# Kernel tuning notes

Hardware: AMD Instinct MI355X
Metric: run time of the kernel (lower is better)

Reference implementation:

```python
import jax, jax.numpy as jnp
import numpy as np

B, C, H, W = 2, 192, 256, 256
HEADS = 6


def _conv1x1(x, w, b):
    # x: [b,ci,h,w], w: [co,ci,1,1], b: [co]
    return jnp.einsum('oi,bihw->bohw', w[:, :, 0, 0], x) + b[None, :, None, None]


def _dwconv3x3(x, w, b):
    # depthwise 3x3, padding=1; x: [b,c,h,w], w: [c,1,3,3], b: [c]
    y = jax.lax.conv_general_dilated(
        x, w, window_strides=(1, 1), padding='SAME',
        feature_group_count=x.shape[1],
        dimension_numbers=('NCHW', 'OIHW', 'NCHW'))
    return y + b[None, :, None, None]


def _l2norm(t, eps=1e-12):
    # F.normalize(dim=-1): x / max(||x||_2, eps)
    n = jnp.sqrt(jnp.sum(t * t, axis=-1, keepdims=True))
    return t / jnp.maximum(n, eps)


def setup_inputs() -> dict:
    key = jax.random.key(0)
    ks = jax.random.split(key, 12)
    s = 0.02
    return {
        'feat_guide': jax.random.normal(ks[0], (B, C, H, W), jnp.float32),
        'feat_op': jax.random.normal(ks[1], (B, C, H, W), jnp.float32),
        'q_w': jax.random.normal(ks[2], (C, C, 1, 1), jnp.float32) * s,
        'q_b': jax.random.normal(ks[3], (C,), jnp.float32) * s,
        'kv_w': jax.random.normal(ks[4], (2 * C, C, 1, 1), jnp.float32) * s,
        'kv_b': jax.random.normal(ks[5], (2 * C,), jnp.float32) * s,
        'q_dw_w': jax.random.normal(ks[6], (C, 1, 3, 3), jnp.float32) * s,
        'q_dw_b': jax.random.normal(ks[7], (C,), jnp.float32) * s,
        'kv_dw_w': jax.random.normal(ks[8], (2 * C, 1, 3, 3), jnp.float32) * s,
        'kv_dw_b': jax.random.normal(ks[9], (2 * C,), jnp.float32) * s,
        'proj_w': jax.random.normal(ks[10], (C, C, 1, 1), jnp.float32) * s,
        'proj_b': jax.random.normal(ks[11], (C,), jnp.float32) * s,
        'temperature': jnp.ones((HEADS, 1, 1), jnp.float32),
    }


def reference(feat_guide, feat_op, q_w, q_b, kv_w, kv_b, q_dw_w, q_dw_b,
              kv_dw_w, kv_dw_b, proj_w, proj_b, temperature):
    b, c, h, w = feat_guide.shape
    q = _dwconv3x3(_conv1x1(feat_guide, q_w, q_b), q_dw_w, q_dw_b)
    kv = _dwconv3x3(_conv1x1(feat_op, kv_w, kv_b), kv_dw_w, kv_dw_b)
    k, v = jnp.split(kv, 2, axis=1)

    def heads(t):  # [b,c,h,w] -> [b,heads,c/heads,hw]
        return t.reshape(b, HEADS, c // HEADS, h * w)

    q = _l2norm(heads(q))
    k = _l2norm(heads(k))
    v = heads(v)
    # channel-wise attention: [b,heads,c',c'] scores over hw
    attn = jnp.einsum('bhcn,bhdn->bhcd', q, k) * temperature[None]
    attn = jax.nn.softmax(attn, axis=-1)
    out = jnp.einsum('bhcd,bhdn->bhcn', attn, v).reshape(b, c, h, w)
    return _conv1x1(out, proj_w, proj_b)
```

## Files before the change

kernel.cpp:

```cpp
#include <hip/hip_runtime.h>

#define HW_N 65536
#define CC 192
#define NCHUNKS 256

typedef __attribute__((ext_vector_type(8))) short short8v;
typedef __attribute__((ext_vector_type(4))) short short4v;
typedef __attribute__((ext_vector_type(4))) float f32x4;
typedef __attribute__((ext_vector_type(4))) int int4v;

__device__ __forceinline__ float bf2f(unsigned short u) {
  union { unsigned int i; float f; } v; v.i = ((unsigned int)u) << 16; return v.f;
}
__device__ __forceinline__ unsigned short f2bf(float f) {
  union { float f; unsigned int i; } v; v.f = f;
  unsigned int r = v.i + 0x7fffu + ((v.i >> 16) & 1u);
  return (unsigned short)(r >> 16);
}

__global__ __launch_bounds__(256) void cvt_w(
    const float* __restrict__ qw, const float* __restrict__ kvw,
    unsigned short* __restrict__ Wq, unsigned short* __restrict__ Wkv) {
  const int i = (blockIdx.x * 256 + threadIdx.x) * 8;
  const float* src; unsigned short* dst; int off;
  if (i < 36864) { src = qw; dst = Wq; off = i; }
  else { src = kvw; dst = Wkv; off = i - 36864; }
  unsigned short tmp[8];
#pragma unroll
  for (int j = 0; j < 8; ++j) tmp[j] = f2bf(src[off + j]);
  *(short8v*)(dst + off) = *(short8v*)tmp;
}

template <int INF32, int OUTF32>
__device__ __forceinline__ void gemm_body(
    const void* __restrict__ X_, const unsigned short* __restrict__ W,
    const float* __restrict__ bias, void* __restrict__ out_,
    int Mtot, int m0, int n0, int b, int t, unsigned char* smem) {
  typedef unsigned short row200[200];
  typedef unsigned short row152[152];
  row200* Bt = (row200*)smem;
  row152* Rp = (row152*)smem;
  const int lane = t & 63, wv = t >> 6;
  const int l15 = lane & 15, lg = lane >> 4;
  const int wm = wv & 3, wn = wv >> 2;
  const int mrow = m0 + wm * 48;
  const int nw = wn * 64;
  const size_t xbase = (size_t)b * CC * (size_t)HW_N + n0;

  for (int task = t; task < 768; task += 512) {
    const int kp = task >> 5, nq = task & 31;
    unsigned int p[8][2];
    if (INF32) {
      const float* Xf = (const float*)X_;
#pragma unroll
      for (int j = 0; j < 8; ++j) {
        f32x4 v = *(const f32x4*)(Xf + xbase + (size_t)(kp * 8 + j) * HW_N + nq * 4);
        p[j][0] = (unsigned int)f2bf(v[0]) | ((unsigned int)f2bf(v[1]) << 16);
        p[j][1] = (unsigned int)f2bf(v[2]) | ((unsigned int)f2bf(v[3]) << 16);
      }
    } else {
      const unsigned short* Xh = (const unsigned short*)X_;
#pragma unroll
      for (int j = 0; j < 8; ++j) {
        short4v v = *(const short4v*)(Xh + xbase + (size_t)(kp * 8 + j) * HW_N + nq * 4);
        p[j][0] = (unsigned int)(unsigned short)v[0] | ((unsigned int)(unsigned short)v[1] << 16);
        p[j][1] = (unsigned int)(unsigned short)v[2] | ((unsigned int)(unsigned short)v[3] << 16);
      }
    }
    const int kpx = kp ^ (nq & 7);
#pragma unroll
    for (int nn = 0; nn < 4; ++nn) {
      unsigned int q4[4];
#pragma unroll
      for (int wi = 0; wi < 4; ++wi) {
        const unsigned int lo = (p[2 * wi][nn >> 1] >> ((nn & 1) * 16)) & 0xffffu;
        const unsigned int hi = (p[2 * wi + 1][nn >> 1] >> ((nn & 1) * 16)) & 0xffffu;
        q4[wi] = lo | (hi << 16);
      }
      *(int4v*)&Bt[nq * 4 + nn][kpx * 8] = *(int4v*)q4;
    }
  }
  __syncthreads();

  f32x4 acc[3][4] = {};
#pragma unroll
  for (int kc = 0; kc < 6; ++kc) {
    const int k0 = kc * 32 + lg * 8;
    short8v af[3], bfr[4];
#pragma unroll
    for (int fr = 0; fr < 3; ++fr)
      af[fr] = *(const short8v*)(W + (size_t)(mrow + fr * 16 + l15) * CC + k0);
#pragma unroll
    for (int fc = 0; fc < 4; ++fc) {
      const int row = nw + fc * 16 + l15;
      const int oct = (kc * 4 + lg) ^ ((row >> 2) & 7);
      bfr[fc] = *(const short8v*)&Bt[row][oct * 8];
    }
#pragma unroll
    for (int fr = 0; fr < 3; ++fr)
#pragma unroll
      for (int fc = 0; fc < 4; ++fc)
        acc[fr][fc] = __builtin_amdgcn_mfma_f32_16x16x32_bf16(af[fr], bfr[fc], acc[fr][fc], 0, 0, 0);
  }

  const size_t obase = (size_t)b * Mtot * (size_t)HW_N;
  if (OUTF32) {
    float* outf = (float*)out_;
#pragma unroll
    for (int fr = 0; fr < 3; ++fr) {
      const int rbase = mrow + fr * 16 + lg * 4;
#pragma unroll
      for (int r = 0; r < 4; ++r) {
        const float bb = bias[rbase + r];
        const size_t ro = obase + (size_t)(rbase + r) * HW_N + n0 + nw;
#pragma unroll
        for (int fc = 0; fc < 4; ++fc)
          outf[ro + fc * 16 + l15] = acc[fr][fc][r] + bb;
      }
    }
    return;
  }
  __syncthreads();

#pragma unroll
  for (int half = 0; half < 2; ++half) {
    if ((wm >> 1) == half) {
      const int mbase = (wm & 1) * 48;
#pragma unroll
      for (int fr = 0; fr < 3; ++fr) {
#pragma unroll
        for (int r = 0; r < 4; ++r) {
          const int mloc = mbase + fr * 16 + lg * 4 + r;
          const float bb = bias[m0 + half * 96 + mloc];
#pragma unroll
          for (int fc = 0; fc < 4; ++fc)
            Rp[mloc][nw + fc * 16 + l15] = f2bf(acc[fr][fc][r] + bb);
        }
      }
    }
    __syncthreads();
#pragma unroll
    for (int s = 0; s < 3; ++s) {
      const int idx = s * 512 + t;
      const int m = idx >> 4, n8 = (idx & 15) * 8;
      short8v v = *(short8v*)&Rp[m][n8];
      const size_t oo = obase + (size_t)(m0 + half * 96 + m) * HW_N + n0 + n8;
      *(short8v*)((unsigned short*)out_ + oo) = v;
    }
    __syncthreads();
  }
}

__global__ __launch_bounds__(512) void conv_gemm_qkv(
    const float* __restrict__ fg, const float* __restrict__ fo,
    const unsigned short* __restrict__ Wq, const unsigned short* __restrict__ Wkv,
    const float* __restrict__ q_b, const float* __restrict__ kv_b,
    unsigned short* __restrict__ QC, unsigned short* __restrict__ KVC) {
  __shared__ __align__(16) unsigned char smem[51200];
  const int d = blockIdx.x;
  const int b = blockIdx.z;
  const int t = threadIdx.x;
  if (d < 512) {
    gemm_body<1, 0>((const void*)fg, Wq, q_b, (void*)QC, 192, 0, d * 128, b, t, smem);
  } else {
    const int dd = d - 512;
    const int mt = (dd >> 3) & 1;
    const int nt = (dd & 7) | ((dd >> 4) << 3);
    gemm_body<1, 0>((const void*)fo, Wkv, kv_b, (void*)KVC, 384, mt * 192, nt * 128, b, t, smem);
  }
}

__global__ __launch_bounds__(512) void conv_gemm_final(
    const unsigned short* __restrict__ Vb, const unsigned short* __restrict__ Mw,
    const float* __restrict__ proj_b, float* __restrict__ out) {
  __shared__ __align__(16) unsigned char smem[51200];
  const int b = blockIdx.z;
  gemm_body<0, 1>((const void*)Vb, Mw + (size_t)b * CC * CC, proj_b, (void*)out,
                  192, 0, blockIdx.x * 128, b, threadIdx.x, smem);
}

__global__ __launch_bounds__(256) void dwconv3x3_all(
    const unsigned short* __restrict__ QC, const unsigned short* __restrict__ KVC,
    const float* __restrict__ q_dw_w, const float* __restrict__ q_dw_b,
    const float* __restrict__ kv_dw_w, const float* __restrict__ kv_dw_b,
    unsigned short* __restrict__ Qb, unsigned short* __restrict__ Kb,
    unsigned short* __restrict__ Vb) {
  const int t = threadIdx.x;
  const int wc = (t & 31) * 8;
  const int h0 = blockIdx.x * 32 + (t >> 5) * 4;
  const int y = blockIdx.y, b = blockIdx.z;
  const unsigned short* in; const float* w; float bv; unsigned short* out;
  if (y < 192) {
    in = QC + ((size_t)b * 192 + y) * (size_t)HW_N;
    w = q_dw_w + y * 9; bv = q_dw_b[y];
    out = Qb + ((size_t)b * 192 + y) * (size_t)HW_N;
  } else if (y < 384) {
    const int c = y - 192;
    in = KVC + ((size_t)b * 384 + c) * (size_t)HW_N;
    w = kv_dw_w + c * 9; bv = kv_dw_b[c];
    out = Kb + ((size_t)b * 192 + c) * (size_t)HW_N;
  } else {
    const int c = y - 384;
    in = KVC + ((size_t)b * 384 + 192 + c) * (size_t)HW_N;
    w = kv_dw_w + (192 + c) * 9; bv = kv_dw_b[192 + c];
    out = Vb + ((size_t)b * 192 + c) * (size_t)HW_N;
  }
  float wv9[9];
#pragma unroll
  for (int i = 0; i < 9; ++i) wv9[i] = w[i];
  float f[6][10];
#pragma unroll
  for (int ky = 0; ky < 6; ++ky) {
    const int hh = h0 + ky - 1;
    if (hh < 0 || hh > 255) {
#pragma unroll
      for (int j = 0; j < 10; ++j) f[ky][j] = 0.f;
    } else {
      const unsigned short* row = in + hh * 256;
      short8v v = *(const short8v*)(row + wc);
      f[ky][0] = (wc > 0) ? bf2f(row[wc - 1]) : 0.f;
#pragma unroll
      for (int j = 0; j < 8; ++j) f[ky][1 + j] = bf2f((unsigned short)v[j]);
      f[ky][9] = (wc < 248) ? bf2f(row[wc + 8]) : 0.f;
    }
  }
#pragma unroll
  for (int rr = 0; rr < 4; ++rr) {
    union { short8v v; unsigned short u[8]; } o;
#pragma unroll
    for (int j = 0; j < 8; ++j) {
      float acc = bv;
#pragma unroll
      for (int ky = 0; ky < 3; ++ky)
#pragma unroll
        for (int kx = 0; kx < 3; ++kx)
          acc += wv9[ky * 3 + kx] * f[rr + ky][j + kx];
      o.u[j] = f2bf(acc);
    }
    *(short8v*)(out + (h0 + rr) * 256 + wc) = o.v;
  }
}

__global__ __launch_bounds__(64) void gram_kernel(
    const unsigned short* __restrict__ Q, const unsigned short* __restrict__ K,
    float* __restrict__ Gp, float* __restrict__ nqp, float* __restrict__ nkp) {
  const int lane = threadIdx.x;
  const int l15 = lane & 15, lg = lane >> 4;
  const int chunk = blockIdx.x, h = blockIdx.y, b = blockIdx.z;
  const int bh = b * 6 + h;
  const size_t base = ((size_t)b * CC + h * 32) * (size_t)HW_N;
  f32x4 acc[2][2] = {};
  float sq[2] = {0.f, 0.f}, sk[2] = {0.f, 0.f};
  const int nst = chunk * 256 + lg * 8;
  for (int ks = 0; ks < 8; ++ks) {
    const int n = nst + ks * 32;
    short8v qa[2], kb[2];
#pragma unroll
    for (int fr = 0; fr < 2; ++fr) {
      qa[fr] = *(const short8v*)(Q + base + (size_t)(fr * 16 + l15) * HW_N + n);
      kb[fr] = *(const short8v*)(K + base + (size_t)(fr * 16 + l15) * HW_N + n);
    }
#pragma unroll
    for (int fr = 0; fr < 2; ++fr)
#pragma unroll
      for (int j = 0; j < 8; ++j) {
        float a = bf2f((unsigned short)qa[fr][j]); sq[fr] += a * a;
        float c2 = bf2f((unsigned short)kb[fr][j]); sk[fr] += c2 * c2;
      }
#pragma unroll
    for (int fr = 0; fr < 2; ++fr)
#pragma unroll
      for (int fc = 0; fc < 2; ++fc)
        acc[fr][fc] = __builtin_amdgcn_mfma_f32_16x16x32_bf16(qa[fr], kb[fc], acc[fr][fc], 0, 0, 0);
  }
  float* Gb = Gp + (size_t)(chunk * 12 + bh) * 1024;
#pragma unroll
  for (int fr = 0; fr < 2; ++fr)
#pragma unroll
    for (int fc = 0; fc < 2; ++fc)
#pragma unroll
      for (int r = 0; r < 4; ++r)
        Gb[(fr * 16 + lg * 4 + r) * 32 + fc * 16 + l15] = acc[fr][fc][r];
#pragma unroll
  for (int fr = 0; fr < 2; ++fr) {
    float v = sq[fr]; v += __shfl_down(v, 32); v += __shfl_down(v, 16);
    float u = sk[fr]; u += __shfl_down(u, 32); u += __shfl_down(u, 16);
    if (lane < 16) {
      nqp[(size_t)(chunk * 12 + bh) * 32 + fr * 16 + lane] = v;
      nkp[(size_t)(chunk * 12 + bh) * 32 + fr * 16 + lane] = u;
    }
  }
}

__global__ __launch_bounds__(256) void attn_proj_fused(
    const float* __restrict__ Gp, const float* __restrict__ nqp, const float* __restrict__ nkp,
    const float* __restrict__ temp, const float* __restrict__ proj_w,
    unsigned short* __restrict__ Mout) {
  const int h = blockIdx.x, b = blockIdx.y;
  const int bh = b * 6 + h;
  const int t = threadIdx.x;
  __shared__ float sc[32][33];
  __shared__ float nrmq[32], nrmk[32];

  f32x4 gs = {0.f, 0.f, 0.f, 0.f};
  const float* gbase = Gp + (size_t)bh * 1024 + t * 4;
  for (int ch = 0; ch < NCHUNKS; ++ch) {
    f32x4 v = *(const f32x4*)(gbase + (size_t)ch * 12288);
    gs[0] += v[0]; gs[1] += v[1]; gs[2] += v[2]; gs[3] += v[3];
  }
  {
    const int c = t >> 3, d0 = (t * 4) & 31;
#pragma unroll
    for (int j = 0; j < 4; ++j) sc[c][d0 + j] = gs[j];
  }
  if (t < 64) {
    const float* np = (t < 32 ? nqp : nkp) + (size_t)bh * 32 + (t & 31);
    float s = 0.f;
    for (int ch = 0; ch < NCHUNKS; ++ch) s += np[(size_t)ch * 384];
    if (t < 32) nrmq[t] = fmaxf(sqrtf(s), 1e-12f);
    else nrmk[t - 32] = fmaxf(sqrtf(s), 1e-12f);
  }
  __syncthreads();
  const float tpr = temp[h];
  for (int i = t; i < 1024; i += 256) {
    const int c = i >> 5, d = i & 31;
    sc[c][d] = sc[c][d] * tpr / (nrmq[c] * nrmk[d]);
  }
  __syncthreads();
  if (t < 32) {
    float mx = -1e30f;
    for (int d = 0; d < 32; ++d) mx = fmaxf(mx, sc[t][d]);
    float sum = 0.f;
    for (int d = 0; d < 32; ++d) { float e = __expf(sc[t][d] - mx); sc[t][d] = e; sum += e; }
    const float inv = 1.f / sum;
    for (int d = 0; d < 32; ++d) sc[t][d] *= inv;
  }
  __syncthreads();
  for (int i = t; i < 6144; i += 256) {
    const int co = i >> 5, d = i & 31;
    float acc = 0.f;
    for (int c = 0; c < 32; ++c) acc += proj_w[co * CC + h * 32 + c] * sc[c][d];
    Mout[((size_t)b * CC + co) * CC + h * 32 + d] = f2bf(acc);
  }
}

extern "C" void kernel_launch(void* const* d_in, const int* in_sizes, int n_in,
                              void* d_out, int out_size, void* d_ws, size_t ws_size,
                              hipStream_t stream) {
  const float* fg = (const float*)d_in[0];
  const float* fo = (const float*)d_in[1];
  const float* q_w = (const float*)d_in[2];
  const float* q_b = (const float*)d_in[3];
  const float* kv_w = (const float*)d_in[4];
  const float* kv_b = (const float*)d_in[5];
  const float* q_dw_w = (const float*)d_in[6];
  const float* q_dw_b = (const float*)d_in[7];
  const float* kv_dw_w = (const float*)d_in[8];
  const float* kv_dw_b = (const float*)d_in[9];
  const float* proj_w = (const float*)d_in[10];
  const float* proj_b = (const float*)d_in[11];
  const float* temp = (const float*)d_in[12];

  char* ws = (char*)d_ws;
  unsigned short* QC  = (unsigned short*)(ws + 0);
  unsigned short* KVC = (unsigned short*)(ws + 50331648);
  unsigned short* Qb  = (unsigned short*)(ws + 150994944);
  unsigned short* Kb  = (unsigned short*)(ws + 0);
  unsigned short* Vb  = (unsigned short*)(ws + 50331648);
  float* Gp  = (float*)(ws + 100663296);
  float* nqp = (float*)(ws + 113246208);
  float* nkp = (float*)(ws + 113639424);
  unsigned short* Mw  = (unsigned short*)(ws + 208063488);
  unsigned short* Wq  = (unsigned short*)(ws + 208210944);
  unsigned short* Wkv = (unsigned short*)(ws + 208284672);

  cvt_w<<<dim3(54), dim3(256), 0, stream>>>(q_w, kv_w, Wq, Wkv);
  conv_gemm_qkv<<<dim3(1536, 1, 2), dim3(512), 0, stream>>>(
      fg, fo, Wq, Wkv, q_b, kv_b, QC, KVC);
  dwconv3x3_all<<<dim3(8, 576, 2), dim3(256), 0, stream>>>(
      QC, KVC, q_dw_w, q_dw_b, kv_dw_w, kv_dw_b, Qb, Kb, Vb);
  gram_kernel<<<dim3(NCHUNKS, 6, 2), dim3(64), 0, stream>>>(Qb, Kb, Gp, nqp, nkp);
  attn_proj_fused<<<dim3(6, 2), dim3(256), 0, stream>>>(
      Gp, nqp, nkp, temp, proj_w, Mw);
  conv_gemm_final<<<dim3(512, 1, 2), dim3(512), 0, stream>>>(Vb, Mw, proj_b, (float*)d_out);
}
```

Baseline: 266.9 us.

## Fuse Q/K depthwise conv into Gram kernel via shared-memory row tiles

Computes the Q and K depthwise 3x3 convolutions for two image rows per block into LDS and feeds them straight into the MFMA Gram and norm accumulation, so the Q and K intermediates are never written to or re-read from global memory. Each block reduces its four wave partials in LDS and writes one partial per row pair, which halves the number of partial chunks. V still gets its own depthwise kernel. The trailing __syncthreads in the GEMM body is skipped on the second half. The costs are that each block rereads its 3-row halo from global memory and that the Gram blocks are much larger, with more LDS and register pressure.

Result: slower. 294.6 us (+10.4%).

```diff
diff --git a/kernel.cpp b/kernel.cpp
--- a/kernel.cpp
+++ b/kernel.cpp
@@ -2,7 +2,7 @@
 
 #define HW_N 65536
 #define CC 192
-#define NCHUNKS 256
+#define GCHUNKS 128
 
 typedef __attribute__((ext_vector_type(8))) short short8v;
 typedef __attribute__((ext_vector_type(4))) short short4v;
@@ -147,7 +147,7 @@
       const size_t oo = obase + (size_t)(m0 + half * 96 + m) * HW_N + n0 + n8;
       *(short8v*)((unsigned short*)out_ + oo) = v;
     }
-    __syncthreads();
+    if (half == 0) __syncthreads();
   }
 }
 
@@ -179,32 +179,17 @@
                   192, 0, blockIdx.x * 128, b, threadIdx.x, smem);
 }
 
-__global__ __launch_bounds__(256) void dwconv3x3_all(
-    const unsigned short* __restrict__ QC, const unsigned short* __restrict__ KVC,
-    const float* __restrict__ q_dw_w, const float* __restrict__ q_dw_b,
-    const float* __restrict__ kv_dw_w, const float* __restrict__ kv_dw_b,
-    unsigned short* __restrict__ Qb, unsigned short* __restrict__ Kb,
-    unsigned short* __restrict__ Vb) {
+__global__ __launch_bounds__(256) void dwconv3x3_v(
+    const unsigned short* __restrict__ KVC, const float* __restrict__ kv_dw_w,
+    const float* __restrict__ kv_dw_b, unsigned short* __restrict__ Vb) {
   const int t = threadIdx.x;
   const int wc = (t & 31) * 8;
   const int h0 = blockIdx.x * 32 + (t >> 5) * 4;
-  const int y = blockIdx.y, b = blockIdx.z;
-  const unsigned short* in; const float* w; float bv; unsigned short* out;
-  if (y < 192) {
-    in = QC + ((size_t)b * 192 + y) * (size_t)HW_N;
-    w = q_dw_w + y * 9; bv = q_dw_b[y];
-    out = Qb + ((size_t)b * 192 + y) * (size_t)HW_N;
-  } else if (y < 384) {
-    const int c = y - 192;
-    in = KVC + ((size_t)b * 384 + c) * (size_t)HW_N;
-    w = kv_dw_w + c * 9; bv = kv_dw_b[c];
-    out = Kb + ((size_t)b * 192 + c) * (size_t)HW_N;
-  } else {
-    const int c = y - 384;
-    in = KVC + ((size_t)b * 384 + 192 + c) * (size_t)HW_N;
-    w = kv_dw_w + (192 + c) * 9; bv = kv_dw_b[192 + c];
-    out = Vb + ((size_t)b * 192 + c) * (size_t)HW_N;
-  }
+  const int c = blockIdx.y, b = blockIdx.z;
+  const unsigned short* in = KVC + ((size_t)b * 384 + 192 + c) * (size_t)HW_N;
+  const float* w = kv_dw_w + (192 + c) * 9;
+  const float bv = kv_dw_b[192 + c];
+  unsigned short* out = Vb + ((size_t)b * CC + c) * (size_t)HW_N;
   float wv9[9];
 #pragma unroll
   for (int i = 0; i < 9; ++i) wv9[i] = w[i];
@@ -241,54 +226,132 @@
   }
 }
 
-__global__ __launch_bounds__(64) void gram_kernel(
-    const unsigned short* __restrict__ Q, const unsigned short* __restrict__ K,
+__global__ __launch_bounds__(256) void dwgram(
+    const unsigned short* __restrict__ QC, const unsigned short* __restrict__ KVC,
+    const float* __restrict__ q_dw_w, const float* __restrict__ q_dw_b,
+    const float* __restrict__ kv_dw_w, const float* __restrict__ kv_dw_b,
     float* __restrict__ Gp, float* __restrict__ nqp, float* __restrict__ nkp) {
-  const int lane = threadIdx.x;
+  __shared__ __align__(16) unsigned char smem[33280];
+  typedef unsigned short row260[260];
+  row260* Qs = (row260*)smem;
+  row260* Ks = (row260*)(smem + 16640);
+  float* Pp = (float*)smem;
+  float* Np = (float*)(smem + 16640);
+  const int t = threadIdx.x;
+  const int rp = blockIdx.x, h = blockIdx.y, b = blockIdx.z;
+  const int bh = b * 6 + h;
+  const int lane = t & 63, wv = t >> 6;
   const int l15 = lane & 15, lg = lane >> 4;
-  const int chunk = blockIdx.x, h = blockIdx.y, b = blockIdx.z;
-  const int bh = b * 6 + h;
-  const size_t base = ((size_t)b * CC + h * 32) * (size_t)HW_N;
+
   f32x4 acc[2][2] = {};
   float sq[2] = {0.f, 0.f}, sk[2] = {0.f, 0.f};
-  const int nst = chunk * 256 + lg * 8;
-  for (int ks = 0; ks < 8; ++ks) {
-    const int n = nst + ks * 32;
-    short8v qa[2], kb[2];
-#pragma unroll
-    for (int fr = 0; fr < 2; ++fr) {
-      qa[fr] = *(const short8v*)(Q + base + (size_t)(fr * 16 + l15) * HW_N + n);
-      kb[fr] = *(const short8v*)(K + base + (size_t)(fr * 16 + l15) * HW_N + n);
-    }
-#pragma unroll
-    for (int fr = 0; fr < 2; ++fr)
+
+  for (int rr2 = 0; rr2 < 2; ++rr2) {
+    const int r = rp * 2 + rr2;
+#pragma unroll
+    for (int it = 0; it < 8; ++it) {
+      const int tid = it * 256 + t;
+      const int tensor = tid >> 10;
+      const int c = (tid >> 5) & 31;
+      const int g = tid & 31;
+      const int ch = h * 32 + c;
+      const unsigned short* src = tensor == 0
+          ? QC + ((size_t)b * CC + ch) * (size_t)HW_N
+          : KVC + ((size_t)b * 384 + ch) * (size_t)HW_N;
+      const float* wp = (tensor == 0 ? q_dw_w : kv_dw_w) + ch * 9;
+      const float bv = (tensor == 0 ? q_dw_b : kv_dw_b)[ch];
+      float wv9[9];
+#pragma unroll
+      for (int i = 0; i < 9; ++i) wv9[i] = wp[i];
+      const int w0 = g * 8;
+      float f[3][10];
+#pragma unroll
+      for (int ky = 0; ky < 3; ++ky) {
+        const int rimg = r + ky - 1;
+        if (rimg < 0 || rimg > 255) {
+#pragma unroll
+          for (int j = 0; j < 10; ++j) f[ky][j] = 0.f;
+        } else {
+          const unsigned short* row = src + rimg * 256;
+          short8v v = *(const short8v*)(row + w0);
+          f[ky][0] = (w0 > 0) ? bf2f(row[w0 - 1]) : 0.f;
+#pragma unroll
+          for (int j = 0; j < 8; ++j) f[ky][1 + j] = bf2f((unsigned short)v[j]);
+          f[ky][9] = (w0 < 248) ? bf2f(row[w0 + 8]) : 0.f;
+        }
+      }
+      union { short8v v; unsigned short u[8]; } o;
 #pragma unroll
       for (int j = 0; j < 8; ++j) {
-        float a = bf2f((unsigned short)qa[fr][j]); sq[fr] += a * a;
-        float c2 = bf2f((unsigned short)kb[fr][j]); sk[fr] += c2 * c2;
-      }
-#pragma unroll
-    for (int fr = 0; fr < 2; ++fr)
-#pragma unroll
-      for (int fc = 0; fc < 2; ++fc)
-        acc[fr][fc] = __builtin_amdgcn_mfma_f32_16x16x32_bf16(qa[fr], kb[fc], acc[fr][fc], 0, 0, 0);
-  }
-  float* Gb = Gp + (size_t)(chunk * 12 + bh) * 1024;
+        float a = bv;
+#pragma unroll
+        for (int ky = 0; ky < 3; ++ky)
+#pragma unroll
+          for (int kx = 0; kx < 3; ++kx)
+            a += wv9[ky * 3 + kx] * f[ky][j + kx];
+        o.u[j] = f2bf(a);
+      }
+      if (tensor == 0) *(short8v*)&Qs[c][w0] = o.v;
+      else *(short8v*)&Ks[c][w0] = o.v;
+    }
+    __syncthreads();
+
+#pragma unroll
+    for (int s = 0; s < 2; ++s) {
+      const int px = (wv * 2 + s) * 32 + lg * 8;
+      short8v qa[2], kb[2];
+#pragma unroll
+      for (int fr = 0; fr < 2; ++fr) {
+        qa[fr] = *(const short8v*)&Qs[fr * 16 + l15][px];
+        kb[fr] = *(const short8v*)&Ks[fr * 16 + l15][px];
+      }
+#pragma unroll
+      for (int fr = 0; fr < 2; ++fr)
+#pragma unroll
+        for (int j = 0; j < 8; ++j) {
+          float a = bf2f((unsigned short)qa[fr][j]); sq[fr] += a * a;
+          float c2 = bf2f((unsigned short)kb[fr][j]); sk[fr] += c2 * c2;
+        }
+#pragma unroll
+      for (int fr = 0; fr < 2; ++fr)
+#pragma unroll
+        for (int fc = 0; fc < 2; ++fc)
+          acc[fr][fc] = __builtin_amdgcn_mfma_f32_16x16x32_bf16(qa[fr], kb[fc], acc[fr][fc], 0, 0, 0);
+    }
+    __syncthreads();
+  }
+
 #pragma unroll
   for (int fr = 0; fr < 2; ++fr)
 #pragma unroll
     for (int fc = 0; fc < 2; ++fc)
 #pragma unroll
-      for (int r = 0; r < 4; ++r)
-        Gb[(fr * 16 + lg * 4 + r) * 32 + fc * 16 + l15] = acc[fr][fc][r];
+      for (int rr = 0; rr < 4; ++rr)
+        Pp[wv * 1024 + (fr * 16 + lg * 4 + rr) * 32 + fc * 16 + l15] = acc[fr][fc][rr];
 #pragma unroll
   for (int fr = 0; fr < 2; ++fr) {
     float v = sq[fr]; v += __shfl_down(v, 32); v += __shfl_down(v, 16);
     float u = sk[fr]; u += __shfl_down(u, 32); u += __shfl_down(u, 16);
     if (lane < 16) {
-      nqp[(size_t)(chunk * 12 + bh) * 32 + fr * 16 + lane] = v;
-      nkp[(size_t)(chunk * 12 + bh) * 32 + fr * 16 + lane] = u;
-    }
+      Np[wv * 64 + fr * 16 + lane] = v;
+      Np[wv * 64 + 32 + fr * 16 + lane] = u;
+    }
+  }
+  __syncthreads();
+
+  {
+    f32x4 s = {0.f, 0.f, 0.f, 0.f};
+#pragma unroll
+    for (int w = 0; w < 4; ++w) {
+      f32x4 v = *(const f32x4*)&Pp[w * 1024 + t * 4];
+      s[0] += v[0]; s[1] += v[1]; s[2] += v[2]; s[3] += v[3];
+    }
+    *(f32x4*)&Gp[(size_t)(rp * 12 + bh) * 1024 + t * 4] = s;
+  }
+  if (t < 64) {
+    const float s = Np[t] + Np[64 + t] + Np[128 + t] + Np[192 + t];
+    if (t < 32) nqp[(size_t)(rp * 12 + bh) * 32 + t] = s;
+    else nkp[(size_t)(rp * 12 + bh) * 32 + (t - 32)] = s;
   }
 }
 
@@ -304,7 +367,7 @@
 
   f32x4 gs = {0.f, 0.f, 0.f, 0.f};
   const float* gbase = Gp + (size_t)bh * 1024 + t * 4;
-  for (int ch = 0; ch < NCHUNKS; ++ch) {
+  for (int ch = 0; ch < GCHUNKS; ++ch) {
     f32x4 v = *(const f32x4*)(gbase + (size_t)ch * 12288);
     gs[0] += v[0]; gs[1] += v[1]; gs[2] += v[2]; gs[3] += v[3];
   }
@@ -316,7 +379,7 @@
   if (t < 64) {
     const float* np = (t < 32 ? nqp : nkp) + (size_t)bh * 32 + (t & 31);
     float s = 0.f;
-    for (int ch = 0; ch < NCHUNKS; ++ch) s += np[(size_t)ch * 384];
+    for (int ch = 0; ch < GCHUNKS; ++ch) s += np[(size_t)ch * 384];
     if (t < 32) nrmq[t] = fmaxf(sqrtf(s), 1e-12f);
     else nrmk[t - 32] = fmaxf(sqrtf(s), 1e-12f);
   }
@@ -364,22 +427,21 @@
   char* ws = (char*)d_ws;
   unsigned short* QC  = (unsigned short*)(ws + 0);
   unsigned short* KVC = (unsigned short*)(ws + 50331648);
-  unsigned short* Qb  = (unsigned short*)(ws + 150994944);
-  unsigned short* Kb  = (unsigned short*)(ws + 0);
-  unsigned short* Vb  = (unsigned short*)(ws + 50331648);
-  float* Gp  = (float*)(ws + 100663296);
-  float* nqp = (float*)(ws + 113246208);
-  float* nkp = (float*)(ws + 113639424);
-  unsigned short* Mw  = (unsigned short*)(ws + 208063488);
-  unsigned short* Wq  = (unsigned short*)(ws + 208210944);
-  unsigned short* Wkv = (unsigned short*)(ws + 208284672);
+  unsigned short* Vb  = (unsigned short*)(ws + 150994944);
+  float* Gp  = (float*)(ws + 201326592);
+  float* nqp = (float*)(ws + 207618048);
+  float* nkp = (float*)(ws + 207814656);
+  unsigned short* Mw  = (unsigned short*)(ws + 208011264);
+  unsigned short* Wq  = (unsigned short*)(ws + 208158720);
+  unsigned short* Wkv = (unsigned short*)(ws + 208232448);
 
   cvt_w<<<dim3(54), dim3(256), 0, stream>>>(q_w, kv_w, Wq, Wkv);
   conv_gemm_qkv<<<dim3(1536, 1, 2), dim3(512), 0, stream>>>(
       fg, fo, Wq, Wkv, q_b, kv_b, QC, KVC);
-  dwconv3x3_all<<<dim3(8, 576, 2), dim3(256), 0, stream>>>(
-      QC, KVC, q_dw_w, q_dw_b, kv_dw_w, kv_dw_b, Qb, Kb, Vb);
-  gram_kernel<<<dim3(NCHUNKS, 6, 2), dim3(64), 0, stream>>>(Qb, Kb, Gp, nqp, nkp);
+  dwgram<<<dim3(GCHUNKS, 6, 2), dim3(256), 0, stream>>>(
+      QC, KVC, q_dw_w, q_dw_b, kv_dw_w, kv_dw_b, Gp, nqp, nkp);
+  dwconv3x3_v<<<dim3(8, 192, 2), dim3(256), 0, stream>>>(
+      KVC, kv_dw_w, kv_dw_b, Vb);
   attn_proj_fused<<<dim3(6, 2), dim3(256), 0, stream>>>(
       Gp, nqp, nkp, temp, proj_w, Mw);
   conv_gemm_final<<<dim3(512, 1, 2), dim3(512), 0, stream>>>(Vb, Mw, proj_b, (float*)d_out);
```

## Specialize QKV conv GEMM with async global-to-LDS double-buffered fp32 loads

Applied to the files above, without the earlier changes.

Replaces the generic gemm_body call in the QKV 1x1-conv kernel with a specialized body. Activation tiles are streamed as fp32 directly into LDS via global_load_lds with an XOR swizzle and two buffers, while weights are read from global memory straight into registers. The fp32-to-bf16 conversion moves into the fragment build, and LDS use drops to 32 KB, which may raise occupancy. It also removes the trailing barrier after the last epilogue half. In exchange, the loop does more per-element conversion work and carries extra barrier pairs per k-chunk.

Measured after the change: 265.4 us. No clear change (-0.6%).

```diff
diff --git a/kernel.cpp b/kernel.cpp
--- a/kernel.cpp
+++ b/kernel.cpp
@@ -147,7 +147,7 @@
       const size_t oo = obase + (size_t)(m0 + half * 96 + m) * HW_N + n0 + n8;
       *(short8v*)((unsigned short*)out_ + oo) = v;
     }
-    __syncthreads();
+    if (half == 0) __syncthreads();
   }
 }
 
@@ -156,17 +156,102 @@
     const unsigned short* __restrict__ Wq, const unsigned short* __restrict__ Wkv,
     const float* __restrict__ q_b, const float* __restrict__ kv_b,
     unsigned short* __restrict__ QC, unsigned short* __restrict__ KVC) {
-  __shared__ __align__(16) unsigned char smem[51200];
+  __shared__ __align__(16) unsigned char smem[32768];
+  typedef unsigned short row152[152];
+  row152* Rp = (row152*)smem;
   const int d = blockIdx.x;
   const int b = blockIdx.z;
   const int t = threadIdx.x;
-  if (d < 512) {
-    gemm_body<1, 0>((const void*)fg, Wq, q_b, (void*)QC, 192, 0, d * 128, b, t, smem);
-  } else {
+  const float* X; const unsigned short* W; const float* bias; unsigned short* out;
+  int Mtot, m0, n0;
+  if (d < 512) { X = fg; W = Wq; bias = q_b; out = QC; Mtot = 192; m0 = 0; n0 = d * 128; }
+  else {
     const int dd = d - 512;
     const int mt = (dd >> 3) & 1;
     const int nt = (dd & 7) | ((dd >> 4) << 3);
-    gemm_body<1, 0>((const void*)fo, Wkv, kv_b, (void*)KVC, 384, mt * 192, nt * 128, b, t, smem);
+    X = fo; W = Wkv; bias = kv_b; out = KVC; Mtot = 384; m0 = mt * 192; n0 = nt * 128;
+  }
+  const int lane = t & 63, wv = t >> 6;
+  const int l15 = lane & 15, lg = lane >> 4;
+  const int wm = wv & 3, wn = wv >> 2;
+  const int mrow = m0 + wm * 48;
+  const int nw = wn * 64;
+  const size_t xbase = (size_t)b * CC * (size_t)HW_N + n0;
+
+  auto issue = [&](int kc) {
+    const int bsel = kc & 1;
+#pragma unroll
+    for (int i = 0; i < 2; ++i) {
+      const int blk = wv * 2 + i;
+      const int kl = blk * 2 + (lane >> 5);
+      const int g = (lane & 31) ^ (((kl >> 3) & 1) << 2);
+      const float* gp = X + xbase + (size_t)(kc * 32 + kl) * HW_N + g * 4;
+      __builtin_amdgcn_global_load_lds(
+          (const __attribute__((address_space(1))) void*)gp,
+          (__attribute__((address_space(3))) void*)(smem + bsel * 16384 + blk * 1024),
+          16, 0, 0);
+    }
+  };
+
+  issue(0);
+  issue(1);
+
+  f32x4 acc[3][4] = {};
+  for (int kc = 0; kc < 6; ++kc) {
+    __syncthreads();
+    const float* buf = (const float*)(smem + (kc & 1) * 16384);
+    short8v af[3], bfr[4];
+    const int k0 = kc * 32 + lg * 8;
+#pragma unroll
+    for (int fr = 0; fr < 3; ++fr)
+      af[fr] = *(const short8v*)(W + (size_t)(mrow + fr * 16 + l15) * CC + k0);
+#pragma unroll
+    for (int fc = 0; fc < 4; ++fc) {
+      const int nn = nw + fc * 16 + l15;
+      const int sg = (((nn >> 2) ^ ((lg & 1) << 2)) << 2) + (nn & 3);
+      unsigned short u[8];
+#pragma unroll
+      for (int j = 0; j < 8; ++j)
+        u[j] = f2bf(buf[(lg * 8 + j) * 128 + sg]);
+      bfr[fc] = *(short8v*)u;
+    }
+    __syncthreads();
+    if (kc < 4) issue(kc + 2);
+#pragma unroll
+    for (int fr = 0; fr < 3; ++fr)
+#pragma unroll
+      for (int fc = 0; fc < 4; ++fc)
+        acc[fr][fc] = __builtin_amdgcn_mfma_f32_16x16x32_bf16(af[fr], bfr[fc], acc[fr][fc], 0, 0, 0);
+  }
+
+  const size_t obase = (size_t)b * Mtot * (size_t)HW_N;
+  __syncthreads();
+#pragma unroll
+  for (int half = 0; half < 2; ++half) {
+    if ((wm >> 1) == half) {
+      const int mbase = (wm & 1) * 48;
+#pragma unroll
+      for (int fr = 0; fr < 3; ++fr) {
+#pragma unroll
+        for (int r = 0; r < 4; ++r) {
+          const int mloc = mbase + fr * 16 + lg * 4 + r;
+          const float bb = bias[m0 + half * 96 + mloc];
+#pragma unroll
+          for (int fc = 0; fc < 4; ++fc)
+            Rp[mloc][nw + fc * 16 + l15] = f2bf(acc[fr][fc][r] + bb);
+        }
+      }
+    }
+    __syncthreads();
+#pragma unroll
+    for (int s = 0; s < 3; ++s) {
+      const int idx = s * 512 + t;
+      const int m = idx >> 4, n8 = (idx & 15) * 8;
+      short8v v = *(short8v*)&Rp[m][n8];
+      const size_t oo = obase + (size_t)(m0 + half * 96 + m) * HW_N + n0 + n8;
+      *(short8v*)(out + oo) = v;
+    }
+    if (half == 0) __syncthreads();
   }
 }
 
```
